# Optimization experiments

Hardware: AMD Instinct MI355X
Metric: run time of the kernel (lower is better)

The kernel has to match this reference:

```python
import jax, jax.numpy as jnp
import numpy as np

NEG_INF = -1e9


def setup_inputs() -> dict:
    key = jax.random.key(0)
    ks = jax.random.split(key, 6)
    B, S, D, H, Dh = 2, 2048, 1024, 16, 64
    scale = 1.0 / np.sqrt(D)
    return {
        "x": jax.random.normal(ks[0], (B, S, D), jnp.float32),
        "W_Q": jax.random.normal(ks[1], (H, D, Dh), jnp.float32) * scale,
        "b_Q": jnp.zeros((H, Dh), jnp.float32),
        "W_K": jax.random.normal(ks[2], (H, D, Dh), jnp.float32) * scale,
        "b_K": jnp.zeros((H, Dh), jnp.float32),
        "W_V": jax.random.normal(ks[3], (H, D, Dh), jnp.float32) * scale,
        "W_O": jax.random.normal(ks[4], (H, Dh, D), jnp.float32) * scale,
        "b_V": jnp.zeros((H, Dh), jnp.float32),
        "b_O": jnp.zeros((H, D), jnp.float32),
    }


def reference(x, W_Q, b_Q, W_K, b_K, W_V, W_O, b_V, b_O):
    # x: [b, s, m]; W_{Q,K,V}: [h, m, d]; W_O: [h, d, m]
    S = x.shape[1]
    d_head = W_Q.shape[-1]

    q = jnp.einsum("bqm,hmd->bqhd", x, W_Q) + b_Q  # [b, q, h, d]
    k = jnp.einsum("bkm,hmd->bkhd", x, W_K) + b_K
    v = jnp.einsum("bkm,hmd->bkhd", x, W_V) + b_V

    scores = jnp.einsum("bqhd,bkhd->bhqk", q, k) / jnp.sqrt(
        jnp.asarray(d_head, x.dtype)
    )  # [b, h, q, k] -- full score matrix, as in the unfused original
    causal = jnp.tril(jnp.ones((S, S), bool))
    scores = jnp.where(causal, scores, jnp.asarray(NEG_INF, x.dtype))
    attn = jax.nn.softmax(scores, axis=-1)

    z = jnp.einsum("bhqk,bkhd->bqhd", attn, v)  # [b, q, h, d]
    # per-head output proj then sum over heads; b_O is [h, m] per the annotation
    out = jnp.einsum("bqhd,hdm->bqm", z, W_O) + jnp.sum(b_O, axis=0)
    return out
```

## Files before the change

### kernel.cpp

```cpp
#include <hip/hip_runtime.h>
#include <cstdint>

typedef unsigned short u16;
typedef short s8v __attribute__((ext_vector_type(8)));
typedef float f4v __attribute__((ext_vector_type(4)));

__device__ __forceinline__ u16 f2b(float f) {
  uint32_t u = __float_as_uint(f);
  u = (u + 0x7FFFu + ((u >> 16) & 1u)) >> 16;
  return (u16)u;
}

__device__ __forceinline__ uint32_t pk2(float a, float b) {
  uint32_t r;
  asm("v_cvt_pk_bf16_f32 %0, %1, %2" : "=v"(r) : "v"(a), "v"(b));
  return r;
}

__device__ __forceinline__ void gload16(const u16* g, u16* l) {
  __builtin_amdgcn_global_load_lds(
      (const __attribute__((address_space(1))) void*)g,
      (__attribute__((address_space(3))) void*)l, 16, 0, 0);
}

__global__ void prep(const float* __restrict__ x, u16* __restrict__ xb,
                     const float* __restrict__ WQ, const float* __restrict__ WK,
                     const float* __restrict__ WV, const float* __restrict__ WO,
                     u16* __restrict__ WTqkv, u16* __restrict__ WOT,
                     const float* __restrict__ bQ, const float* __restrict__ bK,
                     const float* __restrict__ bV, const float* __restrict__ bO,
                     float* __restrict__ bqkv, float* __restrict__ bsum) {
  __shared__ u16 tile[64][65];
  const int bid = blockIdx.x;
  const int tid = threadIdx.x;

  if (bid < 4096) {
    int i = bid * 256 + tid;
    float4 v = ((const float4*)x)[i];
    uint2 o;
    o.x = (uint32_t)f2b(v.x) | ((uint32_t)f2b(v.y) << 16);
    o.y = (uint32_t)f2b(v.z) | ((uint32_t)f2b(v.w) << 16);
    ((uint2*)xb)[i] = o;
  } else if (bid < 4864) {
    int sub = bid - 4096;
    int w = sub >> 8, sub2 = sub & 255;
    const float* W = (w == 0) ? WQ : (w == 1) ? WK : WV;
    u16* dst = WTqkv + (size_t)w * 1024 * 1024;
    const int m0 = (sub2 & 15) * 64;
    const int h  = sub2 >> 4;
    const int c  = tid & 63;
    const int r4 = tid >> 6;
    const float* Wh = W + (size_t)h * 65536;
    for (int i = 0; i < 16; ++i) {
      int lm = i * 4 + r4;
      tile[lm][c] = f2b(Wh[(size_t)(m0 + lm) * 64 + c]);
    }
    __syncthreads();
    for (int i = 0; i < 16; ++i) {
      int dd = i * 4 + r4;
      dst[((size_t)h * 64 + dd) * 1024 + m0 + c] = tile[c][dd];
    }
  } else if (bid < 5120) {
    int sub = bid - 4864;
    const int k0 = (sub & 15) * 64;
    const int m0 = (sub >> 4) * 64;
    const int c  = tid & 63;
    const int r4 = tid >> 6;
    for (int i = 0; i < 16; ++i) {
      int lk = i * 4 + r4;
      tile[lk][c] = f2b(WO[(size_t)(k0 + lk) * 1024 + m0 + c]);
    }
    __syncthreads();
    for (int i = 0; i < 16; ++i) {
      int lm = i * 4 + r4;
      WOT[(size_t)(m0 + lm) * 1024 + k0 + c] = tile[c][lm];
    }
  } else {
    int t = (bid - 5120) * 256 + tid;
    if (t < 1024)       bqkv[t] = bQ[t];
    else if (t < 2048)  bqkv[t] = bK[t - 1024];
    else if (t < 3072)  bqkv[t] = bV[t - 2048];
    else {
      int m = t - 3072;
      float s = 0.f;
      for (int hh = 0; hh < 16; ++hh) s += bO[hh * 1024 + m];
      bsum[m] = s;
    }
  }
}

__global__ void convT_v(const u16* __restrict__ QKV, u16* __restrict__ VT) {
  __shared__ u16 tile[64][65];
  const int r0 = blockIdx.x * 64;
  const int c0 = blockIdx.y * 64;
  const int c  = threadIdx.x & 63;
  const int r4 = threadIdx.x >> 6;
  for (int i = 0; i < 16; ++i) {
    int lr = i * 4 + r4;
    tile[lr][c] = QKV[(size_t)(r0 + lr) * 3072 + 2048 + c0 + c];
  }
  __syncthreads();
  for (int i = 0; i < 16; ++i) {
    int lc = i * 4 + r4;
    VT[(size_t)(c0 + lc) * 4096 + r0 + c] = tile[c][lc];
  }
}

template<bool OUT_F32, int BM, int BN, int NTHR>
__global__ void gemm_bt(const u16* __restrict__ A, const u16* __restrict__ BT,
                        const float* __restrict__ bias, void* __restrict__ Cout,
                        int N, int K, int scale_cols) {
  constexpr int NW = NTHR / 64;
  constexpr int WM = NW / 2;
  constexpr int NJ = BN / 32;
  static_assert(BM / WM == 64, "per-wave rows must be 64");
  static_assert(BM * 4 == 2 * NTHR, "A staging: 2 segs/thread");
  static_assert(BN * 4 == NTHR, "B staging: 1 seg/thread");

  __shared__ __align__(16) u16 sA[2][BM * 32];
  __shared__ __align__(16) u16 sB[2][BN * 32];
  const int tid  = threadIdx.x;
  const int lane = tid & 63, wave = tid >> 6;
  const int wm = wave >> 1, wn = wave & 1;
  const int lq = lane & 15, quad = lane >> 4;
  const int m0 = blockIdx.y * BM, n0 = blockIdx.x * BN;

  f4v acc[4][NJ] = {};

  auto STAGE = [&](int buf, int k0) {
    for (int i = 0; i < 2; ++i) {
      int s = tid + i * NTHR;
      int row = s >> 2, part = s & 3;
      gload16(A + (size_t)(m0 + row) * K + k0 + part * 8, &sA[buf][s * 8]);
    }
    {
      int row = tid >> 2, part = tid & 3;
      gload16(BT + (size_t)(n0 + row) * K + k0 + part * 8, &sB[buf][tid * 8]);
    }
  };

  STAGE(0, 0);
  __syncthreads();
  int cur = 0;
  for (int k0 = 0; k0 < K; k0 += 32) {
    if (k0 + 32 < K) STAGE(cur ^ 1, k0 + 32);
    s8v af[4], bfr[NJ];
    for (int i = 0; i < 4; ++i)
      af[i]  = *(const s8v*)&sA[cur][(wm * 64 + i * 16 + lq) * 32 + quad * 8];
    for (int j = 0; j < NJ; ++j)
      bfr[j] = *(const s8v*)&sB[cur][(wn * (BN / 2) + j * 16 + lq) * 32 + quad * 8];
    for (int i = 0; i < 4; ++i)
      for (int j = 0; j < NJ; ++j)
        acc[i][j] = __builtin_amdgcn_mfma_f32_16x16x32_bf16(af[i], bfr[j], acc[i][j], 0, 0, 0);
    __syncthreads();
    cur ^= 1;
  }

  for (int i = 0; i < 4; ++i)
    for (int j = 0; j < NJ; ++j) {
      int row = m0 + wm * 64 + i * 16 + quad * 4;
      int col = n0 + wn * (BN / 2) + j * 16 + lq;
      float bb = bias[col];
      float sc = (col < scale_cols) ? 0.125f : 1.0f;
      for (int r = 0; r < 4; ++r) {
        float v = (acc[i][j][r] + bb) * sc;
        if (OUT_F32) ((float*)Cout)[(size_t)(row + r) * N + col] = v;
        else         ((u16*)Cout)[(size_t)(row + r) * N + col] = f2b(v);
      }
    }
}

__global__ __launch_bounds__(64, 2) void attn_fwd(const u16* __restrict__ QKV,
                                                  const u16* __restrict__ VT,
                                                  u16* __restrict__ Z) {
  __shared__ __align__(16) u16 sP[2][2][16 * 72];
  const int lane = threadIdx.x;
  const int lq = lane & 15, quad = lane >> 4;

  const int id   = blockIdx.x;
  const int xcd  = id & 7;
  const int slot = id >> 3;
  const int g    = xcd + 8 * (slot >> 6);
  const int s    = slot & 63;
  const int u    = (s < 32) ? (63 - s) : (s - 32);
  const int h = g & 15, b = g >> 4;
  const int qA = u * 32, qB = qA + 16;
  const int nchunk = u / 2 + 1;

  const int RS = 3072;
  const u16* base = QKV + (size_t)b * 2048 * RS;
  const u16* Qb  = base + h * 64;
  const u16* Kb  = base + 1024 + h * 64;
  const u16* VTb = VT + (size_t)h * 64 * 4096 + (size_t)b * 2048;

  s8v qfA0 = *(const s8v*)&Qb[(size_t)(qA + lq) * RS + quad * 8];
  s8v qfA1 = *(const s8v*)&Qb[(size_t)(qA + lq) * RS + 32 + quad * 8];
  s8v qfB0 = *(const s8v*)&Qb[(size_t)(qB + lq) * RS + quad * 8];
  s8v qfB1 = *(const s8v*)&Qb[(size_t)(qB + lq) * RS + 32 + quad * 8];

  f4v zA[4] = {}, zB[4] = {};
  float mA = -3.0e38f, lA = 0.f, mB = -3.0e38f, lB = 0.f;

  s8v kf[8], vf[8];

#define LOADK(c_) do {                                                        \
    const int kk0_ = (c_) * 64;                                               \
    _Pragma("unroll")                                                         \
    for (int i_ = 0; i_ < 4; ++i_) {                                          \
      const u16* kr_ = &Kb[(size_t)(kk0_ + 16 * i_ + lq) * RS + quad * 8];    \
      kf[2 * i_]     = *(const s8v*)kr_;                                      \
      kf[2 * i_ + 1] = *(const s8v*)(kr_ + 32);                               \
    }                                                                         \
  } while (0)

#define LOADV(c_) do {                                                        \
    const int kk0_ = (c_) * 64;                                               \
    _Pragma("unroll")                                                         \
    for (int d_ = 0; d_ < 4; ++d_) {                                          \
      const u16* vr_ = &VTb[(size_t)(d_ * 16 + lq) * 4096 + kk0_ + quad * 8]; \
      vf[d_]     = *(const s8v*)vr_;                                          \
      vf[d_ + 4] = *(const s8v*)(vr_ + 32);                                   \
    }                                                                         \
  } while (0)

  auto SMW = [&](int c, int qt0, float& mrow, float& lsum, f4v (&zacc)[4],
                 u16* sPt, f4v (&sc)[4]) {
    float sv[4][4];
    for (int i = 0; i < 4; ++i)
      for (int r = 0; r < 4; ++r) sv[i][r] = sc[i][r];
    if (c + 1 == nchunk) {
      const int kb = c * 64;
      for (int i = 0; i < 4; ++i)
        for (int r = 0; r < 4; ++r)
          if (kb + 16 * i + quad * 4 + r > qt0 + lq) sv[i][r] = -3.0e38f;
    }
    float lmax = sv[0][0];
    for (int i = 0; i < 4; ++i)
      for (int r = 0; r < 4; ++r) lmax = fmaxf(lmax, sv[i][r]);
    if (!__all(lmax <= mrow + 8.0f)) {
      float t = lmax;
      t = fmaxf(t, __shfl_xor(t, 16, 64));
      t = fmaxf(t, __shfl_xor(t, 32, 64));
      float mnew = fmaxf(mrow, t);
      float al = __expf(mrow - mnew);
      mrow = mnew;
      lsum *= al;
      float alr[4];
      for (int r = 0; r < 4; ++r) alr[r] = __shfl(al, quad * 4 + r, 16);
      for (int dc = 0; dc < 4; ++dc)
        for (int r = 0; r < 4; ++r) zacc[dc][r] *= alr[r];
    }
    float acc = 0.f;
    float p[4][4];
    for (int i = 0; i < 4; ++i)
      for (int r = 0; r < 4; ++r) {
        p[i][r] = __expf(sv[i][r] - mrow);
        acc += p[i][r];
      }
    lsum += acc;
    for (int i = 0; i < 4; ++i) {
      uint2 w;
      w.x = pk2(p[i][0], p[i][1]);
      w.y = pk2(p[i][2], p[i][3]);
      *(uint2*)&sPt[lq * 72 + 16 * i + quad * 4] = w;
    }
  };

#define QK(aA_, aB_) do {                                                     \
    _Pragma("unroll")                                                         \
    for (int i_ = 0; i_ < 4; ++i_) {                                          \
      aA_[i_] = __builtin_amdgcn_mfma_f32_16x16x32_bf16(kf[2*i_],   qfA0, aA_[i_], 0, 0, 0); \
      aA_[i_] = __builtin_amdgcn_mfma_f32_16x16x32_bf16(kf[2*i_+1], qfA1, aA_[i_], 0, 0, 0); \
      aB_[i_] = __builtin_amdgcn_mfma_f32_16x16x32_bf16(kf[2*i_],   qfB0, aB_[i_], 0, 0, 0); \
      aB_[i_] = __builtin_amdgcn_mfma_f32_16x16x32_bf16(kf[2*i_+1], qfB1, aB_[i_], 0, 0, 0); \
    }                                                                         \
  } while (0)

  auto PV = [&](int pb) {
    s8v pA0 = *(const s8v*)&sP[0][pb][lq * 72 + quad * 8];
    s8v pA1 = *(const s8v*)&sP[0][pb][lq * 72 + 32 + quad * 8];
    s8v pB0 = *(const s8v*)&sP[1][pb][lq * 72 + quad * 8];
    s8v pB1 = *(const s8v*)&sP[1][pb][lq * 72 + 32 + quad * 8];
#pragma unroll
    for (int d_ = 0; d_ < 4; ++d_) {
      zA[d_] = __builtin_amdgcn_mfma_f32_16x16x32_bf16(pA0, vf[d_],     zA[d_], 0, 0, 0);
      zA[d_] = __builtin_amdgcn_mfma_f32_16x16x32_bf16(pA1, vf[d_ + 4], zA[d_], 0, 0, 0);
      zB[d_] = __builtin_amdgcn_mfma_f32_16x16x32_bf16(pB0, vf[d_],     zB[d_], 0, 0, 0);
      zB[d_] = __builtin_amdgcn_mfma_f32_16x16x32_bf16(pB1, vf[d_ + 4], zB[d_], 0, 0, 0);
    }
  };

  LOADK(0);
  {
    f4v aA[4] = {}, aB[4] = {};
    __builtin_amdgcn_s_setprio(1);
    QK(aA, aB);
    __builtin_amdgcn_s_setprio(0);
    if (nchunk > 1) LOADK(1);
    LOADV(0);
    SMW(0, qA, mA, lA, zA, sP[0][0], aA);
    SMW(0, qB, mB, lB, zB, sP[1][0], aB);
    asm volatile("" ::: "memory");
  }

  for (int c = 1; c < nchunk; ++c) {
    f4v aA[4] = {}, aB[4] = {};
    __builtin_amdgcn_s_setprio(1);
    QK(aA, aB);
    PV((c + 1) & 1);
    __builtin_amdgcn_s_setprio(0);
    asm volatile("" ::: "memory");
    if (c + 1 < nchunk) LOADK(c + 1);
    LOADV(c);
    SMW(c, qA, mA, lA, zA, sP[0][c & 1], aA);
    SMW(c, qB, mB, lB, zB, sP[1][c & 1], aB);
    asm volatile("" ::: "memory");
  }

  {
    __builtin_amdgcn_s_setprio(1);
    PV((nchunk - 1) & 1);
    __builtin_amdgcn_s_setprio(0);
  }
#undef QK
#undef LOADK
#undef LOADV

  lA += __shfl_xor(lA, 16, 64); lA += __shfl_xor(lA, 32, 64);
  lB += __shfl_xor(lB, 16, 64); lB += __shfl_xor(lB, 32, 64);
  float invA[4], invB[4];
  for (int r = 0; r < 4; ++r) {
    invA[r] = 1.0f / __shfl(lA, quad * 4 + r, 16);
    invB[r] = 1.0f / __shfl(lB, quad * 4 + r, 16);
  }
  for (int dc = 0; dc < 4; ++dc)
    for (int r = 0; r < 4; ++r) {
      size_t rowA = (size_t)b * 2048 + qA + quad * 4 + r;
      size_t rowB = (size_t)b * 2048 + qB + quad * 4 + r;
      Z[rowA * 1024 + h * 64 + dc * 16 + lq] = f2b(zA[dc][r] * invA[r]);
      Z[rowB * 1024 + h * 64 + dc * 16 + lq] = f2b(zB[dc][r] * invB[r]);
    }
}

extern "C" void kernel_launch(void* const* d_in, const int* in_sizes, int n_in,
                              void* d_out, int out_size, void* d_ws, size_t ws_size,
                              hipStream_t stream) {
  const float* x  = (const float*)d_in[0];
  const float* WQ = (const float*)d_in[1];
  const float* bQ = (const float*)d_in[2];
  const float* WK = (const float*)d_in[3];
  const float* bK = (const float*)d_in[4];
  const float* WV = (const float*)d_in[5];
  const float* WO = (const float*)d_in[6];
  const float* bV = (const float*)d_in[7];
  const float* bO = (const float*)d_in[8];
  float* out = (float*)d_out;

  uint8_t* ws = (uint8_t*)d_ws;
  u16*   xb    = (u16*)(ws);
  u16*   VTv   = (u16*)(ws);
  u16*   WTqkv = (u16*)(ws + 8388608);
  u16*   WOT   = (u16*)(ws + 14680064);
  u16*   QKV   = (u16*)(ws + 16777216);
  u16*   Zb    = (u16*)(ws + 41943040);
  float* bqkv  = (float*)(ws + 50331648);
  float* bsum  = (float*)(ws + 50343936);

  prep<<<5136, 256, 0, stream>>>(x, xb, WQ, WK, WV, WO, WTqkv, WOT,
                                 bQ, bK, bV, bO, bqkv, bsum);
  gemm_bt<false, 256, 128, 512><<<dim3(24, 16), 512, 0, stream>>>(
      xb, WTqkv, bqkv, (void*)QKV, 3072, 1024, 1024);
  convT_v<<<dim3(64, 16), 256, 0, stream>>>(QKV, VTv);
  attn_fwd<<<dim3(2048, 1, 1), 64, 0, stream>>>(QKV, VTv, Zb);
  gemm_bt<true, 128, 64, 256><<<dim3(16, 32), 256, 0, stream>>>(
      Zb, WOT, bsum, (void*)out, 1024, 1024, 0);
}
```

Before: 220.7 us.

## Fuse V transpose into QKV GEMM epilogue and shrink QKV tile

Removes the separate convT_v kernel. The QKV GEMM blocks covering V columns now transpose their accumulator tile through shared memory and write V^T directly, skipping the row-major V write. The QKV GEMM also moves from a 256x128 tile with 512 threads to 128x128 with 256 threads, doubling the block count. This saves a launch and a round trip of V through global memory, at the cost of an extra LDS pass and sync in the V-column blocks.

After: 209.7 us. 5.0% less time.

```diff
diff --git a/kernel.cpp b/kernel.cpp
--- a/kernel.cpp
+++ b/kernel.cpp
@@ -89,36 +89,26 @@
   }
 }
 
-__global__ void convT_v(const u16* __restrict__ QKV, u16* __restrict__ VT) {
-  __shared__ u16 tile[64][65];
-  const int r0 = blockIdx.x * 64;
-  const int c0 = blockIdx.y * 64;
-  const int c  = threadIdx.x & 63;
-  const int r4 = threadIdx.x >> 6;
-  for (int i = 0; i < 16; ++i) {
-    int lr = i * 4 + r4;
-    tile[lr][c] = QKV[(size_t)(r0 + lr) * 3072 + 2048 + c0 + c];
-  }
-  __syncthreads();
-  for (int i = 0; i < 16; ++i) {
-    int lc = i * 4 + r4;
-    VT[(size_t)(c0 + lc) * 4096 + r0 + c] = tile[c][lc];
-  }
-}
-
-template<bool OUT_F32, int BM, int BN, int NTHR>
+template<bool OUT_F32, int BM, int BN, int NTHR, bool FUSE_VT>
 __global__ void gemm_bt(const u16* __restrict__ A, const u16* __restrict__ BT,
                         const float* __restrict__ bias, void* __restrict__ Cout,
-                        int N, int K, int scale_cols) {
+                        u16* __restrict__ VTout, int N, int K, int scale_cols) {
   constexpr int NW = NTHR / 64;
   constexpr int WM = NW / 2;
   constexpr int NJ = BN / 32;
+  constexpr int ASEG = BM * 4 / NTHR;
+  constexpr int BSEG = BN * 4 / NTHR;
+  constexpr int STG_U16 = (BM + BN) * 64;
+  constexpr int CT_STRIDE = BM + 8;
+  constexpr int SMEM_U16 = (FUSE_VT && BN * CT_STRIDE > STG_U16)
+                               ? BN * CT_STRIDE : STG_U16;
   static_assert(BM / WM == 64, "per-wave rows must be 64");
-  static_assert(BM * 4 == 2 * NTHR, "A staging: 2 segs/thread");
-  static_assert(BN * 4 == NTHR, "B staging: 1 seg/thread");
-
-  __shared__ __align__(16) u16 sA[2][BM * 32];
-  __shared__ __align__(16) u16 sB[2][BN * 32];
+  static_assert(BM * 4 % NTHR == 0 && BN * 4 % NTHR == 0, "staging divisibility");
+
+  __shared__ __align__(16) u16 smem[SMEM_U16];
+  u16* sA = smem;
+  u16* sB = smem + 2 * BM * 32;
+
   const int tid  = threadIdx.x;
   const int lane = tid & 63, wave = tid >> 6;
   const int wm = wave >> 1, wn = wave & 1;
@@ -128,14 +118,17 @@
   f4v acc[4][NJ] = {};
 
   auto STAGE = [&](int buf, int k0) {
-    for (int i = 0; i < 2; ++i) {
+    for (int i = 0; i < ASEG; ++i) {
       int s = tid + i * NTHR;
       int row = s >> 2, part = s & 3;
-      gload16(A + (size_t)(m0 + row) * K + k0 + part * 8, &sA[buf][s * 8]);
-    }
-    {
-      int row = tid >> 2, part = tid & 3;
-      gload16(BT + (size_t)(n0 + row) * K + k0 + part * 8, &sB[buf][tid * 8]);
+      gload16(A + (size_t)(m0 + row) * K + k0 + part * 8,
+              &sA[buf * BM * 32 + s * 8]);
+    }
+    for (int i = 0; i < BSEG; ++i) {
+      int s = tid + i * NTHR;
+      int row = s >> 2, part = s & 3;
+      gload16(BT + (size_t)(n0 + row) * K + k0 + part * 8,
+              &sB[buf * BN * 32 + s * 8]);
     }
   };
 
@@ -146,14 +139,38 @@
     if (k0 + 32 < K) STAGE(cur ^ 1, k0 + 32);
     s8v af[4], bfr[NJ];
     for (int i = 0; i < 4; ++i)
-      af[i]  = *(const s8v*)&sA[cur][(wm * 64 + i * 16 + lq) * 32 + quad * 8];
+      af[i]  = *(const s8v*)&sA[cur * BM * 32 + (wm * 64 + i * 16 + lq) * 32 + quad * 8];
     for (int j = 0; j < NJ; ++j)
-      bfr[j] = *(const s8v*)&sB[cur][(wn * (BN / 2) + j * 16 + lq) * 32 + quad * 8];
+      bfr[j] = *(const s8v*)&sB[cur * BN * 32 + (wn * (BN / 2) + j * 16 + lq) * 32 + quad * 8];
     for (int i = 0; i < 4; ++i)
       for (int j = 0; j < NJ; ++j)
         acc[i][j] = __builtin_amdgcn_mfma_f32_16x16x32_bf16(af[i], bfr[j], acc[i][j], 0, 0, 0);
     __syncthreads();
     cur ^= 1;
+  }
+
+  if (FUSE_VT && n0 >= 2048) {
+    const int vcol0 = n0 - 2048;
+    u16* ct = smem;
+    for (int i = 0; i < 4; ++i)
+      for (int j = 0; j < NJ; ++j) {
+        int row = wm * 64 + i * 16 + quad * 4;
+        int col = wn * (BN / 2) + j * 16 + lq;
+        float bb = bias[n0 + col];
+        uint2 w;
+        w.x = pk2(acc[i][j][0] + bb, acc[i][j][1] + bb);
+        w.y = pk2(acc[i][j][2] + bb, acc[i][j][3] + bb);
+        *(uint2*)&ct[col * CT_STRIDE + row] = w;
+      }
+    __syncthreads();
+    if (tid < BN * 2) {
+      int cc = tid >> 1, half = tid & 1;
+      const uint4* src = (const uint4*)&ct[cc * CT_STRIDE + half * (BM / 2)];
+      uint4* dst = (uint4*)&VTout[(size_t)(vcol0 + cc) * 4096 + m0 + half * (BM / 2)];
+#pragma unroll
+      for (int k = 0; k < BM / 16; ++k) dst[k] = src[k];
+    }
+    return;
   }
 
   for (int i = 0; i < 4; ++i)
@@ -358,20 +375,19 @@
 
   uint8_t* ws = (uint8_t*)d_ws;
   u16*   xb    = (u16*)(ws);
-  u16*   VTv   = (u16*)(ws);
   u16*   WTqkv = (u16*)(ws + 8388608);
   u16*   WOT   = (u16*)(ws + 14680064);
   u16*   QKV   = (u16*)(ws + 16777216);
   u16*   Zb    = (u16*)(ws + 41943040);
   float* bqkv  = (float*)(ws + 50331648);
   float* bsum  = (float*)(ws + 50343936);
+  u16*   VTv   = (u16*)(ws + 50348032);
 
   prep<<<5136, 256, 0, stream>>>(x, xb, WQ, WK, WV, WO, WTqkv, WOT,
                                  bQ, bK, bV, bO, bqkv, bsum);
-  gemm_bt<false, 256, 128, 512><<<dim3(24, 16), 512, 0, stream>>>(
-      xb, WTqkv, bqkv, (void*)QKV, 3072, 1024, 1024);
-  convT_v<<<dim3(64, 16), 256, 0, stream>>>(QKV, VTv);
+  gemm_bt<false, 128, 128, 256, true><<<dim3(24, 32), 256, 0, stream>>>(
+      xb, WTqkv, bqkv, (void*)QKV, VTv, 3072, 1024, 1024);
   attn_fwd<<<dim3(2048, 1, 1), 64, 0, stream>>>(QKV, VTv, Zb);
-  gemm_bt<true, 128, 64, 256><<<dim3(16, 32), 256, 0, stream>>>(
-      Zb, WOT, bsum, (void*)out, 1024, 1024, 0);
-}
+  gemm_bt<true, 128, 64, 256, false><<<dim3(16, 32), 256, 0, stream>>>(
+      Zb, WOT, bsum, (void*)out, nullptr, 1024, 1024, 0);
+}
```
